# Optimization experiments

Hardware: AMD Instinct MI355X
Metric: run time of the kernel (lower is better)

## Reference

```python
import jax, jax.numpy as jnp
import numpy as np

N = 50000      # nodes
E = 800000     # edges (avg degree 16)
D_IN = 64
D_H = 64


def setup_inputs() -> dict:
    key = jax.random.key(0)
    k = jax.random.split(key, 4)
    x = jax.random.normal(k[0], (N, D_IN), dtype=jnp.float32)
    edge_index = jax.random.randint(k[1], (2, E), 0, N, dtype=jnp.int64)
    W1 = jax.random.normal(k[2], (D_IN, D_H), dtype=jnp.float32) * (1.0 / np.sqrt(D_IN))
    b1 = jnp.zeros((D_H,), dtype=jnp.float32)
    W2 = jax.random.normal(k[3], (D_H, 1), dtype=jnp.float32) * (1.0 / np.sqrt(D_H))
    b2 = jnp.zeros((1,), dtype=jnp.float32)
    return {"x": x, "edge_index": edge_index, "W1": W1, "b1": b1, "W2": W2, "b2": b2}


def gcn_conv(x, src, dst, W, b):
    """PyG-style GCNConv: linear -> symmetric-normalized scatter-aggregate + bias.
    src/dst already include self-loops."""
    n = x.shape[0]
    h = x @ W                                                   # [N, Dout]
    deg = jax.ops.segment_sum(jnp.ones_like(dst, dtype=h.dtype), dst, num_segments=n)
    dinv_sqrt = jnp.where(deg > 0, jax.lax.rsqrt(jnp.maximum(deg, 1e-12)), 0.0)
    norm = dinv_sqrt[src] * dinv_sqrt[dst]                       # [E+N]
    agg = jax.ops.segment_sum(h[src] * norm[:, None], dst, num_segments=n)
    return agg + b


def reference(x, edge_index, W1, b1, W2, b2):
    n = x.shape[0]
    loops = jnp.arange(n, dtype=edge_index.dtype)
    src = jnp.concatenate([edge_index[0], loops])                # add self-loops
    dst = jnp.concatenate([edge_index[1], loops])
    h = jax.nn.relu(gcn_conv(x, src, dst, W1, b1))               # [N, D_H]
    out = gcn_conv(h, src, dst, W2, b2)                          # [N, 1]
    return out.squeeze(-1)                                       # [N]
```

## Files before the change

kernel.cpp:

```cpp
#include <hip/hip_runtime.h>
#include <hip/hip_fp16.h>

#define D 64
#define PW2 256
#define PSH2 8
#define EPB 4096

__global__ void k_cast(const float4* __restrict__ x4, const float* __restrict__ dinv,
                       __half2* __restrict__ xh2, int total4) {
    int i = blockIdx.x * blockDim.x + threadIdx.x;
    if (i < total4) {
        float4 v = x4[i];
        float s = dinv[i >> 4];
        xh2[2 * i]     = __floats2half2_rn(v.x * s, v.y * s);
        xh2[2 * i + 1] = __floats2half2_rn(v.z * s, v.w * s);
    }
}

__global__ __launch_bounds__(256) void k_hist(const int* __restrict__ dst, int E,
                                              int* __restrict__ counts, int NP) {
    extern __shared__ int lh[];
    int t = threadIdx.x, b = blockIdx.x;
    for (int i = t; i < NP; i += 256) lh[i] = 0;
    __syncthreads();
    int base = b * EPB;
#pragma unroll
    for (int k = 0; k < EPB / 256; ++k) {
        int e = base + k * 256 + t;
        if (e < E) atomicAdd(&lh[dst[e] >> PSH2], 1);
    }
    __syncthreads();
    for (int i = t; i < NP; i += 256) counts[(size_t)b * NP + i] = lh[i];
}

__global__ __launch_bounds__(256) void k_scanA(int* __restrict__ counts, int NB, int NP,
                                               int* __restrict__ bin_total) {
    __shared__ int sh[256];
    int t = threadIdx.x, bin = blockIdx.x;
    int v = (t < NB) ? counts[(size_t)t * NP + bin] : 0;
    sh[t] = v;
    __syncthreads();
    for (int off = 1; off < 256; off <<= 1) {
        int u = (t >= off) ? sh[t - off] : 0;
        __syncthreads();
        sh[t] += u;
        __syncthreads();
    }
    if (t < NB) counts[(size_t)t * NP + bin] = sh[t] - v;
    if (t == 255) bin_total[bin] = sh[255];
}

__global__ __launch_bounds__(256) void k_scatter(const int* __restrict__ src,
        const int* __restrict__ dst, int E, const int* __restrict__ counts,
        const int* __restrict__ bin_total, int NP, int* __restrict__ csr_e) {
    __shared__ int bs[256];
    extern __shared__ int cur[];
    int t = threadIdx.x, b = blockIdx.x;
    int v = (t < NP) ? bin_total[t] : 0;
    bs[t] = v;
    __syncthreads();
    for (int off = 1; off < 256; off <<= 1) {
        int u = (t >= off) ? bs[t - off] : 0;
        __syncthreads();
        bs[t] += u;
        __syncthreads();
    }
    if (t < NP) cur[t] = counts[(size_t)b * NP + t] + (bs[t] - v);
    __syncthreads();
    int base = b * EPB;
#pragma unroll
    for (int k = 0; k < EPB / 256; ++k) {
        int e = base + k * 256 + t;
        if (e < E) {
            int s = src[e], d = dst[e];
            int pos = atomicAdd(&cur[d >> PSH2], 1);
            csr_e[pos] = s | ((d & (PW2 - 1)) << 16);
        }
    }
}

__global__ __launch_bounds__(256) void k_sort2(const int* __restrict__ csr_e,
        const int* __restrict__ bin_total, int NP, int n,
        int* __restrict__ csr_src, int* __restrict__ row_ptr,
        float* __restrict__ dinv) {
    __shared__ int bs[256];
    __shared__ int cnt[PW2];
    __shared__ int sh[PW2];
    __shared__ int cursor[PW2];
    __shared__ int s_beg, s_end;
    int t = threadIdx.x, p = blockIdx.x;
    int bv = (t < NP) ? bin_total[t] : 0;
    bs[t] = bv;
    __syncthreads();
    for (int off = 1; off < 256; off <<= 1) {
        int u = (t >= off) ? bs[t - off] : 0;
        __syncthreads();
        bs[t] += u;
        __syncthreads();
    }
    if (t == p) { s_beg = bs[t] - bv; s_end = bs[t]; }
    cnt[t] = 0;
    __syncthreads();
    int beg = s_beg, end = s_end;
    for (int i = beg + t; i < end; i += 256) atomicAdd(&cnt[csr_e[i] >> 16], 1);
    __syncthreads();
    int val = cnt[t];
    sh[t] = val;
    __syncthreads();
    for (int off = 1; off < 256; off <<= 1) {
        int u = (t >= off) ? sh[t - off] : 0;
        __syncthreads();
        sh[t] += u;
        __syncthreads();
    }
    int excl = sh[t] - val;
    cursor[t] = beg + excl;
    int node = p * PW2 + t;
    if (node <= n) {
        row_ptr[node] = beg + excl;
        if (node < n) dinv[node] = rsqrtf((float)(val + 1));
    }
    __syncthreads();
    for (int i = beg + t; i < end; i += 256) {
        int e = csr_e[i];
        int q = atomicAdd(&cursor[e >> 16], 1);
        csr_src[q] = e & 0xFFFF;
    }
}

__global__ __launch_bounds__(256) void k_gather(
        const __half2* __restrict__ xh, const float* __restrict__ dinv,
        const int* __restrict__ row_ptr, const int* __restrict__ csr_src,
        float* __restrict__ agg, int n) {
    int tid = threadIdx.x;
    int wave = tid >> 6, lane = tid & 63;
    int eg = lane >> 3, dg = lane & 7;
    int v = blockIdx.x * 4 + wave;
    if (v >= n) return;
    float dv = dinv[v];
    int beg = row_ptr[v], end = row_ptr[v + 1];

    float4 A = make_float4(0.f, 0.f, 0.f, 0.f);
    float4 B = make_float4(0.f, 0.f, 0.f, 0.f);
    float2 f;
#define ACC16(r)                                                        \
    {   __half2 h0 = *(__half2*)&(r).x, h1 = *(__half2*)&(r).y,         \
                h2 = *(__half2*)&(r).z, h3 = *(__half2*)&(r).w;         \
        f = __half22float2(h0); A.x += f.x; A.y += f.y;                 \
        f = __half22float2(h1); A.z += f.x; A.w += f.y;                 \
        f = __half22float2(h2); B.x += f.x; B.y += f.y;                 \
        f = __half22float2(h3); B.z += f.x; B.w += f.y; }

    if (eg == 0) {
        int4 r = *(const int4*)(xh + (size_t)v * 32 + dg * 4);
        ACC16(r);
    }
    int base = beg;
    for (; base + 16 <= end; base += 16) {
        int u0 = csr_src[base + eg];
        int u1 = csr_src[base + 8 + eg];
        int4 r0 = *(const int4*)(xh + (size_t)u0 * 32 + dg * 4);
        int4 r1 = *(const int4*)(xh + (size_t)u1 * 32 + dg * 4);
        ACC16(r0);
        ACC16(r1);
    }
    for (; base < end; base += 8) {
        int idx = base + eg;
        if (idx < end) {
            int u = csr_src[idx];
            int4 r = *(const int4*)(xh + (size_t)u * 32 + dg * 4);
            ACC16(r);
        }
    }
#undef ACC16
#pragma unroll
    for (int off = 8; off <= 32; off <<= 1) {
        A.x += __shfl_xor(A.x, off, 64); A.y += __shfl_xor(A.y, off, 64);
        A.z += __shfl_xor(A.z, off, 64); A.w += __shfl_xor(A.w, off, 64);
        B.x += __shfl_xor(B.x, off, 64); B.y += __shfl_xor(B.y, off, 64);
        B.z += __shfl_xor(B.z, off, 64); B.w += __shfl_xor(B.w, off, 64);
    }
    if (eg == 0) {
        A.x *= dv; A.y *= dv; A.z *= dv; A.w *= dv;
        B.x *= dv; B.y *= dv; B.z *= dv; B.w *= dv;
        *(float4*)&agg[(size_t)v * D + dg * 8] = A;
        *(float4*)&agg[(size_t)v * D + dg * 8 + 4] = B;
    }
}

#define NPW 16
__global__ __launch_bounds__(256) void k_gemm(
        const float* __restrict__ agg, const float* __restrict__ dinv,
        const float* __restrict__ W1, const float* __restrict__ b1,
        const float* __restrict__ W2, float* __restrict__ sd, int n) {
    __shared__ float lrow[4][D];
    int tid = threadIdx.x;
    int wave = tid >> 6, lane = tid & 63;
    float w1c[D];
#pragma unroll
    for (int d = 0; d < D; ++d) w1c[d] = W1[d * D + lane];
    float b1l = b1[lane], w2l = W2[lane];
    int v0 = (blockIdx.x * 4 + wave) * NPW;
    for (int k = 0; k < NPW; ++k) {
        int v = v0 + k;
        if (v >= n) break;
        lrow[wave][lane] = agg[(size_t)v * D + lane];
        __builtin_amdgcn_wave_barrier();
        float h = b1l;
#pragma unroll
        for (int db = 0; db < D; db += 4) {
            float4 r = *(const float4*)&lrow[wave][db];
            h = fmaf(r.x, w1c[db], h);
            h = fmaf(r.y, w1c[db + 1], h);
            h = fmaf(r.z, w1c[db + 2], h);
            h = fmaf(r.w, w1c[db + 3], h);
        }
        float tt = fmaxf(h, 0.0f) * w2l;
#pragma unroll
        for (int off = 1; off <= 32; off <<= 1) tt += __shfl_xor(tt, off, 64);
        if (lane == 0) sd[v] = tt * dinv[v];
        __builtin_amdgcn_wave_barrier();
    }
}

__global__ __launch_bounds__(256) void k_out(const float* __restrict__ sd,
        const float* __restrict__ dinv, const int* __restrict__ row_ptr,
        const int* __restrict__ csr_src, const float* __restrict__ b2,
        float* __restrict__ out, int n) {
    int t = blockIdx.x * blockDim.x + threadIdx.x;
    int v = t >> 3, r = t & 7;
    if (v >= n) return;
    int beg = row_ptr[v], end = row_ptr[v + 1];
    float a = (r == 0) ? sd[v] : 0.0f;
    for (int i = beg + r; i < end; i += 8) a += sd[csr_src[i]];
    a += __shfl_xor(a, 1, 64);
    a += __shfl_xor(a, 2, 64);
    a += __shfl_xor(a, 4, 64);
    if (r == 0) out[v] = b2[0] + a * dinv[v];
}

extern "C" void kernel_launch(void* const* d_in, const int* in_sizes, int n_in,
                              void* d_out, int out_size, void* d_ws, size_t ws_size,
                              hipStream_t stream) {
    const float* x  = (const float*)d_in[0];
    const int*   ei = (const int*)d_in[1];
    const float* W1 = (const float*)d_in[2];
    const float* b1 = (const float*)d_in[3];
    const float* W2 = (const float*)d_in[4];
    const float* b2 = (const float*)d_in[5];

    int n = in_sizes[0] / D;
    int E = in_sizes[1] / 2;
    const int* src = ei;
    const int* dst = ei + E;

    int NP = (n + PW2 - 1) / PW2;
    int NB = (E + EPB - 1) / EPB;

    char* ws = (char*)d_ws;
    auto take = [&](size_t bytes) {
        char* p = ws;
        ws += (bytes + 255) & ~(size_t)255;
        return p;
    };
    int*     counts    = (int*)take((size_t)NB * NP * sizeof(int));
    int*     bin_total = (int*)take((size_t)NP * sizeof(int));
    int*     csr_e     = (int*)take((size_t)E * sizeof(int));
    int*     csr_src   = (int*)take((size_t)E * sizeof(int));
    int*     row_ptr   = (int*)take((size_t)(n + 1) * sizeof(int));
    float*   dinv      = (float*)take((size_t)n * sizeof(float));
    float*   sd        = (float*)take((size_t)n * sizeof(float));
    float*   agg       = (float*)take((size_t)n * D * sizeof(float));
    __half2* xh        = (__half2*)take((size_t)n * D * sizeof(__half));

    float* out = (float*)d_out;
    size_t ldsNP = (size_t)NP * sizeof(int);

    k_hist<<<NB, 256, ldsNP, stream>>>(dst, E, counts, NP);
    k_scanA<<<NP, 256, 0, stream>>>(counts, NB, NP, bin_total);
    k_scatter<<<NB, 256, ldsNP, stream>>>(src, dst, E, counts, bin_total, NP, csr_e);
    k_sort2<<<NP, 256, 0, stream>>>(csr_e, bin_total, NP, n, csr_src, row_ptr, dinv);

    int total4 = n * D / 4;
    k_cast<<<(total4 + 255) / 256, 256, 0, stream>>>((const float4*)x, dinv, xh, total4);

    k_gather<<<(n + 3) / 4, 256, 0, stream>>>(xh, dinv, row_ptr, csr_src, agg, n);
    k_gemm<<<(n + 4 * NPW - 1) / (4 * NPW), 256, 0, stream>>>(agg, dinv, W1, b1,
                                                              W2, sd, n);
    k_out<<<((size_t)n * 8 + 255) / 256, 256, 0, stream>>>(sd, dinv, row_ptr, csr_src,
                                                           b2, out, n);
}
```

Baseline: 89.17 us.

## Shrink CSR partitions, hoist bin scan into own kernel, fuse cast into sort

```diff
diff --git a/kernel.cpp b/kernel.cpp
--- a/kernel.cpp
+++ b/kernel.cpp
@@ -2,75 +2,77 @@
 #include <hip/hip_fp16.h>
 
 #define D 64
-#define PW2 256
-#define PSH2 8
-#define EPB 4096
-
-__global__ void k_cast(const float4* __restrict__ x4, const float* __restrict__ dinv,
-                       __half2* __restrict__ xh2, int total4) {
-    int i = blockIdx.x * blockDim.x + threadIdx.x;
-    if (i < total4) {
-        float4 v = x4[i];
-        float s = dinv[i >> 4];
-        xh2[2 * i]     = __floats2half2_rn(v.x * s, v.y * s);
-        xh2[2 * i + 1] = __floats2half2_rn(v.z * s, v.w * s);
-    }
-}
-
-__global__ __launch_bounds__(256) void k_hist(const int* __restrict__ dst, int E,
+#define PW2 128
+#define PSH2 7
+#define EPB 2048
+
+__global__ __launch_bounds__(512) void k_hist(const int* __restrict__ dst, int E,
                                               int* __restrict__ counts, int NP) {
     extern __shared__ int lh[];
     int t = threadIdx.x, b = blockIdx.x;
-    for (int i = t; i < NP; i += 256) lh[i] = 0;
+    for (int i = t; i < NP; i += 512) lh[i] = 0;
     __syncthreads();
     int base = b * EPB;
 #pragma unroll
-    for (int k = 0; k < EPB / 256; ++k) {
-        int e = base + k * 256 + t;
+    for (int k = 0; k < EPB / 512; ++k) {
+        int e = base + k * 512 + t;
         if (e < E) atomicAdd(&lh[dst[e] >> PSH2], 1);
     }
     __syncthreads();
-    for (int i = t; i < NP; i += 256) counts[(size_t)b * NP + i] = lh[i];
-}
-
-__global__ __launch_bounds__(256) void k_scanA(int* __restrict__ counts, int NB, int NP,
+    for (int i = t; i < NP; i += 512) counts[(size_t)b * NP + i] = lh[i];
+}
+
+__global__ __launch_bounds__(512) void k_scanA(int* __restrict__ counts, int NB, int NP,
                                                int* __restrict__ bin_total) {
-    __shared__ int sh[256];
+    __shared__ int sh[512];
     int t = threadIdx.x, bin = blockIdx.x;
     int v = (t < NB) ? counts[(size_t)t * NP + bin] : 0;
     sh[t] = v;
     __syncthreads();
-    for (int off = 1; off < 256; off <<= 1) {
+    for (int off = 1; off < 512; off <<= 1) {
         int u = (t >= off) ? sh[t - off] : 0;
         __syncthreads();
         sh[t] += u;
         __syncthreads();
     }
     if (t < NB) counts[(size_t)t * NP + bin] = sh[t] - v;
-    if (t == 255) bin_total[bin] = sh[255];
-}
-
-__global__ __launch_bounds__(256) void k_scatter(const int* __restrict__ src,
+    if (t == 511) bin_total[bin] = sh[511];
+}
+
+__global__ __launch_bounds__(1024) void k_scanB(const int* __restrict__ bin_total, int NP,
+                                                int* __restrict__ bin_base) {
+    __shared__ int sh[1024];
+    int t = threadIdx.x;
+    int i0 = 2 * t, i1 = 2 * t + 1;
+    int v0 = (i0 < NP) ? bin_total[i0] : 0;
+    int v1 = (i1 < NP) ? bin_total[i1] : 0;
+    int s = v0 + v1;
+    sh[t] = s;
+    __syncthreads();
+    for (int off = 1; off < 1024; off <<= 1) {
+        int u = (t >= off) ? sh[t - off] : 0;
+        __syncthreads();
+        sh[t] += u;
+        __syncthreads();
+    }
+    int excl = sh[t] - s;
+    if (i0 < NP) bin_base[i0] = excl;
+    if (i1 < NP) bin_base[i1] = excl + v0;
+    if (t == 1023) bin_base[NP] = sh[1023];
+}
+
+__global__ __launch_bounds__(512) void k_scatter(const int* __restrict__ src,
         const int* __restrict__ dst, int E, const int* __restrict__ counts,
-        const int* __restrict__ bin_total, int NP, int* __restrict__ csr_e) {
-    __shared__ int bs[256];
+        const int* __restrict__ bin_base, int NP, int* __restrict__ csr_e) {
     extern __shared__ int cur[];
     int t = threadIdx.x, b = blockIdx.x;
-    int v = (t < NP) ? bin_total[t] : 0;
-    bs[t] = v;
-    __syncthreads();
-    for (int off = 1; off < 256; off <<= 1) {
-        int u = (t >= off) ? bs[t - off] : 0;
-        __syncthreads();
-        bs[t] += u;
-        __syncthreads();
-    }
-    if (t < NP) cur[t] = counts[(size_t)b * NP + t] + (bs[t] - v);
+    for (int i = t; i < NP; i += 512)
+        cur[i] = counts[(size_t)b * NP + i] + bin_base[i];
     __syncthreads();
     int base = b * EPB;
 #pragma unroll
-    for (int k = 0; k < EPB / 256; ++k) {
-        int e = base + k * 256 + t;
+    for (int k = 0; k < EPB / 512; ++k) {
+        int e = base + k * 512 + t;
         if (e < E) {
             int s = src[e], d = dst[e];
             int pos = atomicAdd(&cur[d >> PSH2], 1);
@@ -79,52 +81,57 @@
     }
 }
 
-__global__ __launch_bounds__(256) void k_sort2(const int* __restrict__ csr_e,
-        const int* __restrict__ bin_total, int NP, int n,
+__global__ __launch_bounds__(512) void k_sort2(const int* __restrict__ csr_e,
+        const int* __restrict__ bin_base, int n,
+        const float4* __restrict__ x4, __half2* __restrict__ xh2,
         int* __restrict__ csr_src, int* __restrict__ row_ptr,
         float* __restrict__ dinv) {
-    __shared__ int bs[256];
     __shared__ int cnt[PW2];
-    __shared__ int sh[PW2];
+    __shared__ int sh[512];
     __shared__ int cursor[PW2];
-    __shared__ int s_beg, s_end;
+    __shared__ float ldv[PW2];
     int t = threadIdx.x, p = blockIdx.x;
-    int bv = (t < NP) ? bin_total[t] : 0;
-    bs[t] = bv;
-    __syncthreads();
-    for (int off = 1; off < 256; off <<= 1) {
-        int u = (t >= off) ? bs[t - off] : 0;
-        __syncthreads();
-        bs[t] += u;
-        __syncthreads();
-    }
-    if (t == p) { s_beg = bs[t] - bv; s_end = bs[t]; }
-    cnt[t] = 0;
-    __syncthreads();
-    int beg = s_beg, end = s_end;
-    for (int i = beg + t; i < end; i += 256) atomicAdd(&cnt[csr_e[i] >> 16], 1);
-    __syncthreads();
-    int val = cnt[t];
+    int beg = bin_base[p], end = bin_base[p + 1];
+    if (t < PW2) cnt[t] = 0;
+    __syncthreads();
+    for (int i = beg + t; i < end; i += 512) atomicAdd(&cnt[csr_e[i] >> 16], 1);
+    __syncthreads();
+    int val = (t < PW2) ? cnt[t] : 0;
     sh[t] = val;
     __syncthreads();
-    for (int off = 1; off < 256; off <<= 1) {
+    for (int off = 1; off < 512; off <<= 1) {
         int u = (t >= off) ? sh[t - off] : 0;
         __syncthreads();
         sh[t] += u;
         __syncthreads();
     }
     int excl = sh[t] - val;
-    cursor[t] = beg + excl;
-    int node = p * PW2 + t;
-    if (node <= n) {
-        row_ptr[node] = beg + excl;
-        if (node < n) dinv[node] = rsqrtf((float)(val + 1));
-    }
-    __syncthreads();
-    for (int i = beg + t; i < end; i += 256) {
+    if (t < PW2) {
+        cursor[t] = beg + excl;
+        int node = p * PW2 + t;
+        float dv = rsqrtf((float)(val + 1));
+        ldv[t] = dv;
+        if (node <= n) {
+            row_ptr[node] = beg + excl;
+            if (node < n) dinv[node] = dv;
+        }
+    }
+    __syncthreads();
+    for (int i = beg + t; i < end; i += 512) {
         int e = csr_e[i];
         int q = atomicAdd(&cursor[e >> 16], 1);
         csr_src[q] = e & 0xFFFF;
+    }
+    for (int i = t; i < PW2 * 16; i += 512) {
+        int row = i >> 4;
+        int node = p * PW2 + row;
+        if (node < n) {
+            int gi = node * 16 + (i & 15);
+            float4 v = x4[gi];
+            float s = ldv[row];
+            xh2[2 * gi]     = __floats2half2_rn(v.x * s, v.y * s);
+            xh2[2 * gi + 1] = __floats2half2_rn(v.z * s, v.w * s);
+        }
     }
 }
 
@@ -265,6 +272,7 @@
     };
     int*     counts    = (int*)take((size_t)NB * NP * sizeof(int));
     int*     bin_total = (int*)take((size_t)NP * sizeof(int));
+    int*     bin_base  = (int*)take((size_t)(NP + 1) * sizeof(int));
     int*     csr_e     = (int*)take((size_t)E * sizeof(int));
     int*     csr_src   = (int*)take((size_t)E * sizeof(int));
     int*     row_ptr   = (int*)take((size_t)(n + 1) * sizeof(int));
@@ -276,13 +284,12 @@
     float* out = (float*)d_out;
     size_t ldsNP = (size_t)NP * sizeof(int);
 
-    k_hist<<<NB, 256, ldsNP, stream>>>(dst, E, counts, NP);
-    k_scanA<<<NP, 256, 0, stream>>>(counts, NB, NP, bin_total);
-    k_scatter<<<NB, 256, ldsNP, stream>>>(src, dst, E, counts, bin_total, NP, csr_e);
-    k_sort2<<<NP, 256, 0, stream>>>(csr_e, bin_total, NP, n, csr_src, row_ptr, dinv);
-
-    int total4 = n * D / 4;
-    k_cast<<<(total4 + 255) / 256, 256, 0, stream>>>((const float4*)x, dinv, xh, total4);
+    k_hist<<<NB, 512, ldsNP, stream>>>(dst, E, counts, NP);
+    k_scanA<<<NP, 512, 0, stream>>>(counts, NB, NP, bin_total);
+    k_scanB<<<1, 1024, 0, stream>>>(bin_total, NP, bin_base);
+    k_scatter<<<NB, 512, ldsNP, stream>>>(src, dst, E, counts, bin_base, NP, csr_e);
+    k_sort2<<<NP, 512, 0, stream>>>(csr_e, bin_base, n, (const float4*)x, xh,
+                                    csr_src, row_ptr, dinv);
 
     k_gather<<<(n + 3) / 4, 256, 0, stream>>>(xh, dinv, row_ptr, csr_src, agg, n);
     k_gemm<<<(n + 4 * NPW - 1) / (4 * NPW), 256, 0, stream>>>(agg, dinv, W1, b1,
```

New measurement: 83.99 us. 5.8% less time.
